# Optimization experiments

Measured on AMD Instinct MI355X. Metric: run time of the kernel, lower is better.

Reference implementation:

```python
import jax, jax.numpy as jnp
import numpy as np

B, S, C, E, H, D, V, K = 1024, 64, 512, 16, 1024, 256, 100, 2
NUM_NUM = 32  # num_numerical; categorical positions are S-NUM_NUM


def setup_inputs() -> dict:
    key = jax.random.key(0)
    ks = jax.random.split(key, 20)
    s = 0.02
    return {
        "codec": jax.random.normal(ks[0], (B, C), jnp.float32),
        "mask_pos": jax.random.randint(ks[1], (B, S), 0, 2, jnp.int32),
        "pos_emb": jax.random.normal(ks[2], (S, C), jnp.float32),
        "type_emb": jax.random.normal(ks[3], (2, C), jnp.float32),
        "gW1": jax.random.normal(ks[4], (3 * C + 1, 256), jnp.float32) * s,
        "gb1": jnp.zeros((256,), jnp.float32),
        "gW2": jax.random.normal(ks[5], (256, E), jnp.float32) * s,
        "gb2": jnp.zeros((E,), jnp.float32),
        "eW0": jax.random.normal(ks[6], (E, C, H), jnp.float32) * s,
        "eb0": jnp.zeros((E, H), jnp.float32),
        "eW1": jax.random.normal(ks[7], (E, H, H), jnp.float32) * s,
        "eb1": jnp.zeros((E, H), jnp.float32),
        "eW2": jax.random.normal(ks[8], (E, H, D), jnp.float32) * s,
        "eb2": jnp.zeros((E, D), jnp.float32),
        "nW": jax.random.normal(ks[9], (NUM_NUM, D), jnp.float32) * s,
        "nb": jnp.zeros((NUM_NUM,), jnp.float32),
        "cW": jax.random.normal(ks[10], (S - NUM_NUM, D, V), jnp.float32) * s,
        "cb": jnp.zeros((S - NUM_NUM, V), jnp.float32),
    }


def reference(codec, mask_pos, pos_emb, type_emb, gW1, gb1, gW2, gb2,
              eW0, eb0, eW1, eb1, eW2, eb2, nW, nb, cW, cb):
    maskf = mask_pos.astype(codec.dtype)  # [B,S]
    positions = jnp.arange(S)
    is_cat = (positions >= NUM_NUM).astype(jnp.int32)
    # gate input: [B,S,3C+1]
    gate_in = jnp.concatenate([
        jnp.broadcast_to(codec[:, None, :], (B, S, C)),
        jnp.broadcast_to(pos_emb[None], (B, S, C)),
        jnp.broadcast_to(type_emb[is_cat][None], (B, S, C)),
        maskf[..., None],
    ], axis=-1)
    h = jax.nn.gelu(gate_in @ gW1 + gb1, approximate=False)
    gate_logits = (h @ gW2 + gb2) * maskf[..., None]  # [B,S,E]
    topg, topi = jax.lax.top_k(gate_logits, K)  # [B,S,K]
    gates = jax.nn.softmax(topg, axis=-1)
    # all expert outputs on codec: [E,B,D]
    h0 = jax.nn.leaky_relu(jnp.einsum('bc,ech->ebh', codec, eW0) + eb0[:, None, :])
    h1 = jax.nn.leaky_relu(jnp.einsum('ebh,ehg->ebg', h0, eW1) + eb1[:, None, :])
    eout = jnp.einsum('ebg,egd->ebd', h1, eW2) + eb2[:, None, :]
    # per-token gather: tok[b,s,k,:] = eout[topi[b,s,k], b, :]
    eout_b = eout.transpose(1, 0, 2)  # [B,E,D]
    tok = jnp.take_along_axis(eout_b[:, None, :, :], topi[..., None], axis=2)  # [B,S,K,D]
    combined = jnp.einsum('bsk,bskd->bsd', gates, tok)  # [B,S,D]
    num_recon = jnp.einsum('bnd,nd->bn', combined[:, :NUM_NUM], nW) + nb  # [B,32]
    cat_recon = jnp.einsum('bnd,ndv->bnv', combined[:, NUM_NUM:], cW) + cb  # [B,32,V]
    return num_recon, cat_recon, gates, topi, mask_pos
```

## Files before the change

kernel.cpp:

```cpp
#include <hip/hip_runtime.h>
#include <hip/hip_bf16.h>

typedef __bf16 bf16x8 __attribute__((ext_vector_type(8)));
typedef float f32x4 __attribute__((ext_vector_type(4)));

static constexpr int B_ = 1024, S_ = 64, C_ = 512, E_ = 16, H_ = 1024, D_ = 256, V_ = 100;
static constexpr int NUMN = 32;

__device__ __forceinline__ unsigned short f2bf(float f) {
  union { float f; unsigned u; } x; x.f = f;
  unsigned r = x.u + 0x7fffu + ((x.u >> 16) & 1u);
  return (unsigned short)(r >> 16);
}

__device__ __forceinline__ float erf_fast(float x) {
  float ax = fabsf(x);
  float t = 1.0f / fmaf(0.3275911f, ax, 1.0f);
  float p = fmaf(1.061405429f, t, -1.453152027f);
  p = fmaf(p, t, 1.421413741f);
  p = fmaf(p, t, -0.284496736f);
  p = fmaf(p, t, 0.254829592f);
  p = p * t;
  float e = 1.0f - p * __expf(-ax * ax);
  return copysignf(e, x);
}

__global__ __launch_bounds__(256) void k_codec_bf(const float* __restrict__ src,
                                                  unsigned short* __restrict__ dst, int n) {
  int i = blockIdx.x * 256 + threadIdx.x;
  if (i < n) dst[i] = f2bf(src[i]);
}

__global__ __launch_bounds__(256) void k_transpose_bf(const float* __restrict__ W,
                                                      unsigned short* __restrict__ WT,
                                                      int K, int N) {
  __shared__ float t[32][33];
  int e = blockIdx.z;
  const float* We = W + (size_t)e * K * N;
  unsigned short* Te = WT + (size_t)e * N * K;
  int n0 = blockIdx.x * 32, k0 = blockIdx.y * 32;
  int tx = threadIdx.x & 31, ty = threadIdx.x >> 5;
#pragma unroll
  for (int i = 0; i < 32; i += 8) t[ty + i][tx] = We[(size_t)(k0 + ty + i) * N + n0 + tx];
  __syncthreads();
#pragma unroll
  for (int i = 0; i < 32; i += 8)
    Te[(size_t)(n0 + ty + i) * K + k0 + tx] = f2bf(t[tx][ty + i]);
}

__global__ __launch_bounds__(256) void k_cwt(const float* __restrict__ cW,
                                             unsigned short* __restrict__ cwt) {
  __shared__ float t[32][33];
  int n = blockIdx.z;
  const float* src = cW + (size_t)n * D_ * V_;
  unsigned short* dst = cwt + (size_t)n * 128 * 256;
  int v0 = blockIdx.x * 32, d0 = blockIdx.y * 32;
  int tx = threadIdx.x & 31, ty = threadIdx.x >> 5;
#pragma unroll
  for (int i = 0; i < 32; i += 8) {
    int v = v0 + tx;
    t[ty + i][tx] = (v < V_) ? src[(size_t)(d0 + ty + i) * V_ + v] : 0.f;
  }
  __syncthreads();
#pragma unroll
  for (int i = 0; i < 32; i += 8)
    dst[(size_t)(v0 + ty + i) * 256 + d0 + tx] = f2bf(t[tx][ty + i]);
}

__global__ __launch_bounds__(256) void k_cvt64(const float* __restrict__ gW2,
                                               const float* __restrict__ gW1,
                                               double* __restrict__ w2d,
                                               double* __restrict__ w1ld,
                                               int* __restrict__ flagcnt) {
  int i = blockIdx.x * 256 + threadIdx.x;
  if (i < 4096) w2d[i] = (double)gW2[i];
  if (i < 256) w1ld[i] = (double)gW1[(size_t)(3 * C_) * 256 + i];
  if (i == 0) *flagcnt = 0;
}

__global__ __launch_bounds__(256) void k_codecpart(const float* __restrict__ codec,
                                                   const float* __restrict__ gW1,
                                                   double* __restrict__ cp) {
  int j = threadIdx.x, b = blockIdx.x;
  const float* cb = codec + (size_t)b * C_;
  double a0 = 0, a1 = 0, a2 = 0, a3 = 0;
  for (int k = 0; k < C_; k += 4) {
    a0 += (double)cb[k] * (double)gW1[(size_t)k * 256 + j];
    a1 += (double)cb[k + 1] * (double)gW1[(size_t)(k + 1) * 256 + j];
    a2 += (double)cb[k + 2] * (double)gW1[(size_t)(k + 2) * 256 + j];
    a3 += (double)cb[k + 3] * (double)gW1[(size_t)(k + 3) * 256 + j];
  }
  cp[(size_t)b * 256 + j] = (a0 + a1) + (a2 + a3);
}

__global__ __launch_bounds__(256) void k_postype_part(const float* __restrict__ pos_emb,
                                                      const float* __restrict__ type_emb,
                                                      const float* __restrict__ gW1,
                                                      double* __restrict__ pp) {
  int j = threadIdx.x;
  int s = blockIdx.x;
  int kc = blockIdx.y;
  int tt = (s >= NUMN) ? 1 : 0;
  double a0 = 0, a1 = 0;
  int k0 = kc * 32;
  for (int kk = 0; kk < 32; kk += 2) {
    int k = k0 + kk;
    a0 += (double)pos_emb[(size_t)s * C_ + k] * (double)gW1[(size_t)(C_ + k) * 256 + j] +
          (double)type_emb[(size_t)tt * C_ + k] * (double)gW1[(size_t)(2 * C_ + k) * 256 + j];
    a1 += (double)pos_emb[(size_t)s * C_ + k + 1] * (double)gW1[(size_t)(C_ + k + 1) * 256 + j] +
          (double)type_emb[(size_t)tt * C_ + k + 1] * (double)gW1[(size_t)(2 * C_ + k + 1) * 256 + j];
  }
  pp[((size_t)kc * 64 + s) * 256 + j] = a0 + a1;
}

__global__ __launch_bounds__(256) void k_postype_red(const double* __restrict__ pp,
                                                     const float* __restrict__ gb1,
                                                     double* __restrict__ ptT) {
  int j = threadIdx.x;
  int s = blockIdx.x;
  double acc = (double)gb1[j];
#pragma unroll
  for (int kc = 0; kc < 16; ++kc) acc += pp[((size_t)kc * 64 + s) * 256 + j];
  ptT[(size_t)j * 64 + s] = acc;
}

__global__ __launch_bounds__(256) void k_gate(const double* __restrict__ cp,
                                              const double* __restrict__ ptT,
                                              const float* __restrict__ gW2,
                                              const double* __restrict__ w1ld,
                                              const float* __restrict__ gb2,
                                              const int* __restrict__ mask,
                                              float* __restrict__ out_g,
                                              float* __restrict__ out_i,
                                              float* __restrict__ out_m,
                                              float* __restrict__ tg,
                                              int* __restrict__ ti,
                                              int* __restrict__ flagcnt,
                                              int* __restrict__ flaglist) {
  __shared__ float red[3][64][17];
  int b = blockIdx.x;
  int s = threadIdx.x & 63;
  int wv = __builtin_amdgcn_readfirstlane(threadIdx.x >> 6);
  int token = b * 64 + s;
  double mf = (double)mask[token];
  const double* cpb = cp + (size_t)b * 256;
  float acc[16];
#pragma unroll
  for (int e = 0; e < 16; ++e) acc[e] = 0.f;
#pragma unroll 2
  for (int jj = 0; jj < 64; ++jj) {
    int j = wv * 64 + jj;
    double xd = cpb[j] + ptT[(size_t)j * 64 + s] + mf * w1ld[j];
    float x = (float)xd;
    float ef = erf_fast(x * 0.70710678f);
    float h = 0.5f * x * (1.0f + ef);
    const float* w2 = gW2 + (size_t)j * 16;
#pragma unroll
    for (int e = 0; e < 16; ++e) acc[e] = fmaf(h, w2[e], acc[e]);
  }
  if (wv > 0) {
#pragma unroll
    for (int e = 0; e < 16; ++e) red[wv - 1][s][e] = acc[e];
  }
  __syncthreads();
  if (wv == 0) {
    double vp[16];
#pragma unroll
    for (int e = 0; e < 16; ++e)
      vp[e] = (double)((acc[e] + red[0][s][e]) + (red[1][s][e] + red[2][s][e])) + (double)gb2[e];
    double margin;
    if (mf == 0.0) {
      double mn = 1e300;
#pragma unroll
      for (int e = 0; e < 16; ++e) mn = fmin(mn, fabs(vp[e]));
      margin = mn;
    } else {
      double t1 = -1e300, t2 = -1e300, t3 = -1e300;
#pragma unroll
      for (int e = 0; e < 16; ++e) {
        double v = vp[e];
        if (v > t1) { t3 = t2; t2 = t1; t1 = v; }
        else if (v > t2) { t3 = t2; t2 = v; }
        else if (v > t3) { t3 = v; }
      }
      margin = fmin(t1 - t2, t2 - t3);
    }
    if (margin < 1e-4) {
      int idx = atomicAdd(flagcnt, 1);
      if (idx < 8192) flaglist[idx] = token;
    }
    double v1, v2;
    int i1, i2;
    if (mf == 0.0) {
      int idx[2];
      int c = 0;
      for (int e = 0; e < 16 && c < 2; ++e)
        if (vp[e] > 0.0) idx[c++] = e;
      for (int e = 0; e < 16 && c < 2; ++e)
        if (!(vp[e] > 0.0)) idx[c++] = e;
      i1 = idx[0];
      i2 = idx[1];
      v1 = 0.0;
      v2 = 0.0;
    } else {
      v1 = -1e300; v2 = -1e300; i1 = 0; i2 = 1;
#pragma unroll
      for (int e = 0; e < 16; ++e) {
        double v = vp[e];
        if (v > v1) { v2 = v1; i2 = i1; v1 = v; i1 = e; }
        else if (v > v2) { v2 = v; i2 = e; }
      }
    }
    double ex = exp(v2 - v1);
    double den = 1.0 + ex;
    float g1 = (float)(1.0 / den), g2 = (float)(ex / den);
    out_g[(size_t)token * 2] = g1;
    out_g[(size_t)token * 2 + 1] = g2;
    out_i[(size_t)token * 2] = (float)i1;
    out_i[(size_t)token * 2 + 1] = (float)i2;
    out_m[token] = (float)mf;
    tg[(size_t)token * 2] = g1;
    tg[(size_t)token * 2 + 1] = g2;
    ti[(size_t)token * 2] = i1;
    ti[(size_t)token * 2 + 1] = i2;
  }
}

__global__ __launch_bounds__(64) void k_gate_fix(const double* __restrict__ cp,
                                                 const double* __restrict__ ptT,
                                                 const double* __restrict__ w2d,
                                                 const double* __restrict__ w1ld,
                                                 const float* __restrict__ gb2,
                                                 const int* __restrict__ mask,
                                                 const int* __restrict__ flagcnt,
                                                 const int* __restrict__ flaglist,
                                                 float* __restrict__ out_g,
                                                 float* __restrict__ out_i,
                                                 float* __restrict__ out_m,
                                                 float* __restrict__ tg,
                                                 int* __restrict__ ti) {
  int cnt = *flagcnt;
  if (cnt > 8192) cnt = 8192;
  int lane = threadIdx.x;
  for (int fi = blockIdx.x; fi < cnt; fi += gridDim.x) {
    int token = flaglist[fi];
    int b = token >> 6, sf = token & 63;
    double mf = (double)mask[token];
    const double* cpb = cp + (size_t)b * 256;
    double facc[16];
#pragma unroll
    for (int e = 0; e < 16; ++e) facc[e] = 0.0;
#pragma unroll
    for (int jj = 0; jj < 4; ++jj) {
      int j = jj * 64 + lane;
      double x = cpb[j] + ptT[(size_t)j * 64 + sf] + mf * w1ld[j];
      double h = 0.5 * x * (1.0 + erf(x * 0.70710678118654752440));
      const double* w2 = w2d + (size_t)j * 16;
#pragma unroll
      for (int e = 0; e < 16; ++e) facc[e] += h * w2[e];
    }
#pragma unroll
    for (int off = 32; off >= 1; off >>= 1) {
#pragma unroll
      for (int e = 0; e < 16; ++e) facc[e] += __shfl_xor(facc[e], off, 64);
    }
    if (lane == 0) {
      double vp[16];
#pragma unroll
      for (int e = 0; e < 16; ++e) vp[e] = facc[e] + (double)gb2[e];
      double v1, v2;
      int i1, i2;
      if (mf == 0.0) {
        int idx[2];
        int c = 0;
        for (int e = 0; e < 16 && c < 2; ++e)
          if (vp[e] > 0.0) idx[c++] = e;
        for (int e = 0; e < 16 && c < 2; ++e)
          if (!(vp[e] > 0.0)) idx[c++] = e;
        i1 = idx[0];
        i2 = idx[1];
        v1 = 0.0;
        v2 = 0.0;
      } else {
        v1 = -1e300; v2 = -1e300; i1 = 0; i2 = 1;
#pragma unroll
        for (int e = 0; e < 16; ++e) {
          double v = vp[e];
          if (v > v1) { v2 = v1; i2 = i1; v1 = v; i1 = e; }
          else if (v > v2) { v2 = v; i2 = e; }
        }
      }
      double ex = exp(v2 - v1);
      double den = 1.0 + ex;
      float g1 = (float)(1.0 / den), g2 = (float)(ex / den);
      out_g[(size_t)token * 2] = g1;
      out_g[(size_t)token * 2 + 1] = g2;
      out_i[(size_t)token * 2] = (float)i1;
      out_i[(size_t)token * 2 + 1] = (float)i2;
      out_m[token] = (float)mf;
      tg[(size_t)token * 2] = g1;
      tg[(size_t)token * 2 + 1] = g2;
      ti[(size_t)token * 2] = i1;
      ti[(size_t)token * 2 + 1] = i2;
    }
  }
}

__global__ __launch_bounds__(512, 2) void k_gemm256(const unsigned short* __restrict__ A, size_t aStride,
                                                    const unsigned short* __restrict__ WT,
                                                    const float* __restrict__ bias,
                                                    unsigned short* __restrict__ Out,
                                                    int M, int N, int K) {
  extern __shared__ char lds[];
  char* sA = lds;
  char* sB = lds + 65536;
  int id = blockIdx.x + gridDim.x * (blockIdx.y + gridDim.y * blockIdx.z);
  int e = (id & 7) * 2 + ((id >> 3) & 1);
  int tile = id >> 4;
  int m0 = (tile & 3) * 256, n0 = (tile >> 2) * 256;
  const unsigned short* Ae = A + (size_t)e * aStride;
  const unsigned short* We = WT + (size_t)e * (size_t)N * K;
  int tid = threadIdx.x, lane = tid & 63, w = tid >> 6;
  int l15 = lane & 15, l4 = lane >> 4;
  int r = w >> 2;
  int cc = (w & 3) * 64;
  int hc = cc >> 7;
  int cr = cc & 127;
  f32x4 acc[2][4][4] = {};
  int nk = K >> 6;

  auto stageA = [&](int buf, int h, int kt) {
#pragma unroll
    for (int c = 0; c < 2; ++c) {
      int off = (tid + c * 512) * 16;
      int row = off >> 7;
      int ss = ((off >> 4) & 7) ^ (row & 7);
      const char* src = (const char*)(Ae + (size_t)(m0 + h * 128 + row) * K + kt * 64) + ss * 16;
      __builtin_amdgcn_global_load_lds((const __attribute__((address_space(1))) void*)src,
          (__attribute__((address_space(3))) void*)(sA + buf * 32768 + h * 16384 + off), 16, 0, 0);
    }
  };
  auto stageB = [&](int buf, int h, int kt) {
#pragma unroll
    for (int c = 0; c < 2; ++c) {
      int off = (tid + c * 512) * 16;
      int row = off >> 7;
      int ss = ((off >> 4) & 7) ^ (row & 7);
      const char* src = (const char*)(We + (size_t)(n0 + h * 128 + row) * K + kt * 64) + ss * 16;
      __builtin_amdgcn_global_load_lds((const __attribute__((address_space(1))) void*)src,
          (__attribute__((address_space(3))) void*)(sB + buf * 32768 + h * 16384 + off), 16, 0, 0);
    }
  };
  auto ldA = [&](int buf, int m2, int mi, int ks) {
    int hrow = m2 * 64 + mi * 16 + l15;
    int sp = (l4 + ks * 4) ^ (hrow & 7);
    return *(const bf16x8*)(sA + buf * 32768 + r * 16384 + hrow * 128 + sp * 16);
  };
  auto ldB = [&](int buf, int ni, int ks) {
    int hrow = cr + ni * 16 + l15;
    int sp = (l4 + ks * 4) ^ (hrow & 7);
    return *(const bf16x8*)(sB + buf * 32768 + hc * 16384 + hrow * 128 + sp * 16);
  };

  stageA(0, 0, 0); stageA(0, 1, 0); stageB(0, 0, 0); stageB(0, 1, 0);
  asm volatile("s_waitcnt vmcnt(0)" ::: "memory");
  __builtin_amdgcn_s_barrier();

  for (int t = 0; t < nk; ++t) {
    int cur = t & 1, nxt = cur ^ 1;
    if (t + 1 < nk) {
      stageA(nxt, 0, t + 1); stageA(nxt, 1, t + 1);
      stageB(nxt, 0, t + 1); stageB(nxt, 1, t + 1);
    }
#pragma unroll
    for (int ks = 0; ks < 2; ++ks) {
      bf16x8 bfr[4];
#pragma unroll
      for (int ni = 0; ni < 4; ++ni) bfr[ni] = ldB(cur, ni, ks);
#pragma unroll
      for (int m2 = 0; m2 < 2; ++m2) {
        bf16x8 afr[4];
#pragma unroll
        for (int mi = 0; mi < 4; ++mi) afr[mi] = ldA(cur, m2, mi, ks);
        __builtin_amdgcn_s_setprio(1);
#pragma unroll
        for (int mi = 0; mi < 4; ++mi)
#pragma unroll
          for (int ni = 0; ni < 4; ++ni)
            acc[m2][mi][ni] = __builtin_amdgcn_mfma_f32_16x16x32_bf16(afr[mi], bfr[ni], acc[m2][mi][ni], 0, 0, 0);
        __builtin_amdgcn_s_setprio(0);
      }
    }
    asm volatile("s_waitcnt vmcnt(0)" ::: "memory");
    __builtin_amdgcn_s_barrier();
  }

  size_t obase = (size_t)e * (size_t)M * N;
#pragma unroll
  for (int m2 = 0; m2 < 2; ++m2)
#pragma unroll
    for (int mi = 0; mi < 4; ++mi)
#pragma unroll
      for (int ni = 0; ni < 4; ++ni) {
        int col = n0 + cc + ni * 16 + l15;
        float bv = bias[(size_t)e * N + col];
#pragma unroll
        for (int j = 0; j < 4; ++j) {
          int row = m0 + r * 128 + m2 * 64 + mi * 16 + l4 * 4 + j;
          float v = acc[m2][mi][ni][j] + bv;
          v = (v > 0.f) ? v : 0.01f * v;
          Out[obase + (size_t)row * N + col] = f2bf(v);
        }
      }
}

template <int ACT, int OBF>
__global__ __launch_bounds__(256) void k_gemm(const unsigned short* __restrict__ A, size_t aStride,
                                              const unsigned short* __restrict__ WT,
                                              const float* __restrict__ bias,
                                              void* __restrict__ Out,
                                              int M, int N, int K) {
  __shared__ __align__(16) unsigned short sA[128 * 32];
  __shared__ __align__(16) unsigned short sB[128 * 32];
  int e = blockIdx.z;
  int m0 = blockIdx.x * 128, n0 = blockIdx.y * 128;
  const unsigned short* Ae = A + (size_t)e * aStride;
  const unsigned short* We = WT + (size_t)e * (size_t)N * K;
  int tid = threadIdx.x, lane = tid & 63, w = tid >> 6;
  int l15 = lane & 15, kh = (lane >> 4) * 8;
  int rsub = lane >> 2;
  int kk = (lane & 3) * 8;
  int wr = (w >> 1) * 64, wc = (w & 1) * 64;
  f32x4 acc[4][4] = {};
  int nk = K >> 5;

  auto stage = [&](int kt) {
#pragma unroll
    for (int c = 0; c < 2; ++c) {
      int chunk = w * 2 + c;
      int row = chunk * 16 + rsub;
      const unsigned short* ga = Ae + (size_t)(m0 + row) * K + kt * 32 + kk;
      __builtin_amdgcn_global_load_lds((const __attribute__((address_space(1))) void*)ga,
                                       (__attribute__((address_space(3))) void*)(&sA[chunk * 512]),
                                       16, 0, 0);
      const unsigned short* gb = We + (size_t)(n0 + row) * K + kt * 32 + kk;
      __builtin_amdgcn_global_load_lds((const __attribute__((address_space(1))) void*)gb,
                                       (__attribute__((address_space(3))) void*)(&sB[chunk * 512]),
                                       16, 0, 0);
    }
  };

  stage(0);
  for (int kt = 0; kt < nk; ++kt) {
    __syncthreads();
    bf16x8 a[4], bb[4];
#pragma unroll
    for (int mi = 0; mi < 4; ++mi)
      a[mi] = *(const bf16x8*)&sA[(wr + mi * 16 + l15) * 32 + kh];
#pragma unroll
    for (int ni = 0; ni < 4; ++ni)
      bb[ni] = *(const bf16x8*)&sB[(wc + ni * 16 + l15) * 32 + kh];
#pragma unroll
    for (int mi = 0; mi < 4; ++mi)
#pragma unroll
      for (int ni = 0; ni < 4; ++ni)
        acc[mi][ni] = __builtin_amdgcn_mfma_f32_16x16x32_bf16(a[mi], bb[ni], acc[mi][ni], 0, 0, 0);
    if (kt + 1 < nk) {
      __syncthreads();
      stage(kt + 1);
    }
  }

  unsigned short* outb = (unsigned short*)Out;
  float* outf = (float*)Out;
  size_t obase = (size_t)e * (size_t)M * N;
#pragma unroll
  for (int mi = 0; mi < 4; ++mi) {
#pragma unroll
    for (int ni = 0; ni < 4; ++ni) {
      int col = n0 + wc + ni * 16 + l15;
      float bv = bias[(size_t)e * N + col];
#pragma unroll
      for (int j = 0; j < 4; ++j) {
        int row = m0 + wr + mi * 16 + (lane >> 4) * 4 + j;
        float v = acc[mi][ni][j] + bv;
        if (ACT) v = (v > 0.f) ? v : 0.01f * v;
        if (OBF) outb[obase + (size_t)row * N + col] = f2bf(v);
        else outf[obase + (size_t)row * N + col] = v;
      }
    }
  }
}

__global__ __launch_bounds__(256) void k_comb(const float* __restrict__ eout,
                                              const float* __restrict__ tg,
                                              const int* __restrict__ ti,
                                              unsigned short* __restrict__ combbf) {
  int b = blockIdx.x, n = blockIdx.y, d = threadIdx.x;
  int tk = b * 64 + 32 + n;
  float g1 = tg[(size_t)tk * 2], g2 = tg[(size_t)tk * 2 + 1];
  int i1 = ti[(size_t)tk * 2], i2 = ti[(size_t)tk * 2 + 1];
  float v = g1 * eout[((size_t)i1 * B_ + b) * D_ + d] + g2 * eout[((size_t)i2 * B_ + b) * D_ + d];
  combbf[((size_t)n * B_ + b) * D_ + d] = f2bf(v);
}

__global__ __launch_bounds__(256) void k_catgemm(const unsigned short* __restrict__ combbf,
                                                 const unsigned short* __restrict__ cwt,
                                                 const float* __restrict__ cb,
                                                 float* __restrict__ out1) {
  __shared__ __align__(16) unsigned short sA[128 * 32];
  __shared__ __align__(16) unsigned short sB[128 * 32];
  int n = blockIdx.z;
  int m0 = blockIdx.x * 128;
  const unsigned short* Ae = combbf + (size_t)n * B_ * D_;
  const unsigned short* We = cwt + (size_t)n * 128 * 256;
  int tid = threadIdx.x, lane = tid & 63, w = tid >> 6;
  int l15 = lane & 15, kh = (lane >> 4) * 8;
  int rsub = lane >> 2;
  int kk = (lane & 3) * 8;
  int wr = (w >> 1) * 64, wc = (w & 1) * 64;
  f32x4 acc[4][4] = {};
  const int K = 256, nk = K >> 5;

  auto stage = [&](int kt) {
#pragma unroll
    for (int c = 0; c < 2; ++c) {
      int chunk = w * 2 + c;
      int row = chunk * 16 + rsub;
      const unsigned short* ga = Ae + (size_t)(m0 + row) * K + kt * 32 + kk;
      __builtin_amdgcn_global_load_lds((const __attribute__((address_space(1))) void*)ga,
                                       (__attribute__((address_space(3))) void*)(&sA[chunk * 512]),
                                       16, 0, 0);
      const unsigned short* gb = We + (size_t)row * K + kt * 32 + kk;
      __builtin_amdgcn_global_load_lds((const __attribute__((address_space(1))) void*)gb,
                                       (__attribute__((address_space(3))) void*)(&sB[chunk * 512]),
                                       16, 0, 0);
    }
  };

  stage(0);
  for (int kt = 0; kt < nk; ++kt) {
    __syncthreads();
    bf16x8 a[4], bb[4];
#pragma unroll
    for (int mi = 0; mi < 4; ++mi)
      a[mi] = *(const bf16x8*)&sA[(wr + mi * 16 + l15) * 32 + kh];
#pragma unroll
    for (int ni = 0; ni < 4; ++ni)
      bb[ni] = *(const bf16x8*)&sB[(wc + ni * 16 + l15) * 32 + kh];
#pragma unroll
    for (int mi = 0; mi < 4; ++mi)
#pragma unroll
      for (int ni = 0; ni < 4; ++ni)
        acc[mi][ni] = __builtin_amdgcn_mfma_f32_16x16x32_bf16(a[mi], bb[ni], acc[mi][ni], 0, 0, 0);
    if (kt + 1 < nk) {
      __syncthreads();
      stage(kt + 1);
    }
  }

#pragma unroll
  for (int mi = 0; mi < 4; ++mi) {
#pragma unroll
    for (int ni = 0; ni < 4; ++ni) {
      int col = wc + ni * 16 + l15;
      if (col < V_) {
        float bv = cb[(size_t)n * V_ + col];
#pragma unroll
        for (int j = 0; j < 4; ++j) {
          int row = m0 + wr + mi * 16 + (lane >> 4) * 4 + j;
          out1[((size_t)row * 32 + n) * V_ + col] = acc[mi][ni][j] + bv;
        }
      }
    }
  }
}

__global__ __launch_bounds__(256) void k_num(const float* __restrict__ eout,
                                             const float* __restrict__ nW,
                                             const float* __restrict__ nb,
                                             const float* __restrict__ tg,
                                             const int* __restrict__ ti,
                                             float* __restrict__ out0) {
  int b = blockIdx.x;
  int lane = threadIdx.x & 63;
  int wv = threadIdx.x >> 6;
#pragma unroll
  for (int q = 0; q < 8; ++q) {
    int n = wv * 8 + q;
    int tk = b * 64 + n;
    float g1 = tg[(size_t)tk * 2], g2 = tg[(size_t)tk * 2 + 1];
    int i1 = ti[(size_t)tk * 2], i2 = ti[(size_t)tk * 2 + 1];
    const float4* p1 = (const float4*)(eout + ((size_t)i1 * B_ + b) * D_);
    const float4* p2 = (const float4*)(eout + ((size_t)i2 * B_ + b) * D_);
    const float4* wp = (const float4*)(nW + (size_t)n * D_);
    float4 a = p1[lane], c = p2[lane], ww = wp[lane];
    float acc = fmaf(g1, a.x, g2 * c.x) * ww.x + fmaf(g1, a.y, g2 * c.y) * ww.y +
                fmaf(g1, a.z, g2 * c.z) * ww.z + fmaf(g1, a.w, g2 * c.w) * ww.w;
#pragma unroll
    for (int off = 32; off >= 1; off >>= 1) acc += __shfl_xor(acc, off, 64);
    if (lane == 0) out0[(size_t)b * 32 + n] = nb[n] + acc;
  }
}

extern "C" void kernel_launch(void* const* d_in, const int* in_sizes, int n_in,
                              void* d_out, int out_size, void* d_ws, size_t ws_size,
                              hipStream_t stream) {
  const float* codec = (const float*)d_in[0];
  const int* maskp = (const int*)d_in[1];
  const float* pos_emb = (const float*)d_in[2];
  const float* type_emb = (const float*)d_in[3];
  const float* gW1 = (const float*)d_in[4];
  const float* gb1 = (const float*)d_in[5];
  const float* gW2 = (const float*)d_in[6];
  const float* gb2 = (const float*)d_in[7];
  const float* eW0 = (const float*)d_in[8];
  const float* eb0 = (const float*)d_in[9];
  const float* eW1 = (const float*)d_in[10];
  const float* eb1 = (const float*)d_in[11];
  const float* eW2 = (const float*)d_in[12];
  const float* eb2 = (const float*)d_in[13];
  const float* nW = (const float*)d_in[14];
  const float* nb = (const float*)d_in[15];
  const float* cW = (const float*)d_in[16];
  const float* cb = (const float*)d_in[17];

  char* ws = (char*)d_ws;
  size_t o = 0;
  unsigned short* codecbf = (unsigned short*)(ws + o); o += (size_t)B_ * C_ * 2;
  size_t o_w0t = o;
  unsigned short* w0t = (unsigned short*)(ws + o); o += (size_t)E_ * H_ * C_ * 2;
  unsigned short* w1t = (unsigned short*)(ws + o); o += (size_t)E_ * H_ * H_ * 2;
  unsigned short* w2t = (unsigned short*)(ws + o); o += (size_t)E_ * D_ * H_ * 2;
  size_t o_h0 = o;
  unsigned short* h0 = (unsigned short*)(ws + o); o += (size_t)E_ * B_ * H_ * 2;
  unsigned short* h1 = (unsigned short*)(ws + o); o += (size_t)E_ * B_ * H_ * 2;
  double* cp = (double*)(ws + o); o += (size_t)B_ * 256 * 8;
  double* ptT = (double*)(ws + o); o += (size_t)S_ * 256 * 8;
  float* tg = (float*)(ws + o); o += (size_t)B_ * S_ * 2 * 4;
  int* ti = (int*)(ws + o); o += (size_t)B_ * S_ * 2 * 4;
  double* w2d = (double*)(ws + o); o += 4096 * 8;
  double* w1ld = (double*)(ws + o); o += 256 * 8;
  unsigned short* cwt = (unsigned short*)(ws + o); o += (size_t)32 * 128 * 256 * 2;
  double* pp = (double*)(ws + o); o += (size_t)16 * 64 * 256 * 8;
  int* flagcnt = (int*)(ws + o); o += 256;
  int* flaglist = (int*)(ws + o); o += 8192 * 4;
  float* eout = (float*)(ws + o_w0t);
  unsigned short* combbf = (unsigned short*)(ws + o_h0);

  float* out = (float*)d_out;
  float* out_num = out;
  float* out_cat = out + 32768;
  float* out_g = out + 32768 + 3276800;
  float* out_i = out_g + (size_t)B_ * S_ * 2;
  float* out_m = out_i + (size_t)B_ * S_ * 2;

  hipLaunchKernelGGL(k_codec_bf, dim3((B_ * C_) / 256), dim3(256), 0, stream, codec, codecbf, B_ * C_);
  hipLaunchKernelGGL(k_cvt64, dim3(16), dim3(256), 0, stream, gW2, gW1, w2d, w1ld, flagcnt);
  hipLaunchKernelGGL(k_transpose_bf, dim3(H_ / 32, C_ / 32, E_), dim3(256), 0, stream, eW0, w0t, C_, H_);
  hipLaunchKernelGGL(k_transpose_bf, dim3(H_ / 32, H_ / 32, E_), dim3(256), 0, stream, eW1, w1t, H_, H_);
  hipLaunchKernelGGL(k_transpose_bf, dim3(D_ / 32, H_ / 32, E_), dim3(256), 0, stream, eW2, w2t, H_, D_);
  hipLaunchKernelGGL(k_cwt, dim3(4, 8, 32), dim3(256), 0, stream, cW, cwt);
  hipLaunchKernelGGL(k_codecpart, dim3(B_), dim3(256), 0, stream, codec, gW1, cp);
  hipLaunchKernelGGL(k_postype_part, dim3(S_, 16), dim3(256), 0, stream, pos_emb, type_emb, gW1, pp);
  hipLaunchKernelGGL(k_postype_red, dim3(S_), dim3(256), 0, stream, pp, gb1, ptT);
  hipLaunchKernelGGL(k_gate, dim3(B_), dim3(256), 0, stream, cp, ptT, gW2, w1ld, gb2,
                     maskp, out_g, out_i, out_m, tg, ti, flagcnt, flaglist);
  hipLaunchKernelGGL(k_gate_fix, dim3(2048), dim3(64), 0, stream, cp, ptT, w2d, w1ld, gb2,
                     maskp, flagcnt, flaglist, out_g, out_i, out_m, tg, ti);
  hipLaunchKernelGGL(k_gemm256, dim3(4, 4, E_), dim3(512), 131072, stream,
                     codecbf, (size_t)0, w0t, eb0, h0, 1024, 1024, 512);
  hipLaunchKernelGGL(k_gemm256, dim3(4, 4, E_), dim3(512), 131072, stream,
                     h0, (size_t)(B_ * H_), w1t, eb1, h1, 1024, 1024, 1024);
  hipLaunchKernelGGL((k_gemm<0, 0>), dim3(8, 2, E_), dim3(256), 0, stream,
                     h1, (size_t)(B_ * H_), w2t, eb2, (void*)eout, 1024, 256, 1024);
  hipLaunchKernelGGL(k_comb, dim3(B_, 32), dim3(256), 0, stream, eout, tg, ti, combbf);
  hipLaunchKernelGGL(k_num, dim3(B_), dim3(256), 0, stream, eout, nW, nb, tg, ti, out_num);
  hipLaunchKernelGGL(k_catgemm, dim3(8, 1, 32), dim3(256), 0, stream, combbf, cwt, cb, out_cat);
}
```

Baseline: 230.0 us.

## Switch expert GEMM to triple-buffered K=32 pipeline with partial vmcnt waits

The 256x256 expert GEMM kernel now stages K-tiles of 32 instead of 64 and keeps three LDS buffers in flight, prefetching two tiles ahead. It waits with vmcnt(4) rather than draining all loads each iteration, so global-to-LDS copies can overlap MFMA work. LDS use falls from 128KB to 96KB and launch bounds change to one block per CU. The trade-off is twice as many barriers per K step and a swizzle pattern that only spans 4 slots, which may raise LDS bank conflicts.

```diff
diff --git a/kernel.cpp b/kernel.cpp
--- a/kernel.cpp
+++ b/kernel.cpp
@@ -306,14 +306,12 @@
   }
 }
 
-__global__ __launch_bounds__(512, 2) void k_gemm256(const unsigned short* __restrict__ A, size_t aStride,
+__global__ __launch_bounds__(512, 1) void k_gemm256(const unsigned short* __restrict__ A, size_t aStride,
                                                     const unsigned short* __restrict__ WT,
                                                     const float* __restrict__ bias,
                                                     unsigned short* __restrict__ Out,
                                                     int M, int N, int K) {
   extern __shared__ char lds[];
-  char* sA = lds;
-  char* sB = lds + 65536;
   int id = blockIdx.x + gridDim.x * (blockIdx.y + gridDim.y * blockIdx.z);
   int e = (id & 7) * 2 + ((id >> 3) & 1);
   int tile = id >> 4;
@@ -324,75 +322,71 @@
   int l15 = lane & 15, l4 = lane >> 4;
   int r = w >> 2;
   int cc = (w & 3) * 64;
-  int hc = cc >> 7;
-  int cr = cc & 127;
   f32x4 acc[2][4][4] = {};
-  int nk = K >> 6;
-
-  auto stageA = [&](int buf, int h, int kt) {
+  int nk = K >> 5;
+
+  auto stageA = [&](int buf, int kt) {
 #pragma unroll
     for (int c = 0; c < 2; ++c) {
       int off = (tid + c * 512) * 16;
-      int row = off >> 7;
-      int ss = ((off >> 4) & 7) ^ (row & 7);
-      const char* src = (const char*)(Ae + (size_t)(m0 + h * 128 + row) * K + kt * 64) + ss * 16;
+      int row = off >> 6;
+      int ss = ((off >> 4) & 3) ^ (row & 3);
+      const char* src = (const char*)(Ae + (size_t)(m0 + row) * K + kt * 32) + ss * 16;
       __builtin_amdgcn_global_load_lds((const __attribute__((address_space(1))) void*)src,
-          (__attribute__((address_space(3))) void*)(sA + buf * 32768 + h * 16384 + off), 16, 0, 0);
+          (__attribute__((address_space(3))) void*)(lds + buf * 32768 + off), 16, 0, 0);
     }
   };
-  auto stageB = [&](int buf, int h, int kt) {
+  auto stageB = [&](int buf, int kt) {
 #pragma unroll
     for (int c = 0; c < 2; ++c) {
       int off = (tid + c * 512) * 16;
-      int row = off >> 7;
-      int ss = ((off >> 4) & 7) ^ (row & 7);
-      const char* src = (const char*)(We + (size_t)(n0 + h * 128 + row) * K + kt * 64) + ss * 16;
+      int row = off >> 6;
+      int ss = ((off >> 4) & 3) ^ (row & 3);
+      const char* src = (const char*)(We + (size_t)(n0 + row) * K + kt * 32) + ss * 16;
       __builtin_amdgcn_global_load_lds((const __attribute__((address_space(1))) void*)src,
-          (__attribute__((address_space(3))) void*)(sB + buf * 32768 + h * 16384 + off), 16, 0, 0);
+          (__attribute__((address_space(3))) void*)(lds + buf * 32768 + 16384 + off), 16, 0, 0);
     }
   };
-  auto ldA = [&](int buf, int m2, int mi, int ks) {
-    int hrow = m2 * 64 + mi * 16 + l15;
-    int sp = (l4 + ks * 4) ^ (hrow & 7);
-    return *(const bf16x8*)(sA + buf * 32768 + r * 16384 + hrow * 128 + sp * 16);
+  auto ldA = [&](int buf, int m2, int mi) {
+    int hrow = r * 128 + m2 * 64 + mi * 16 + l15;
+    int sp = l4 ^ (hrow & 3);
+    return *(const bf16x8*)(lds + buf * 32768 + hrow * 64 + sp * 16);
   };
-  auto ldB = [&](int buf, int ni, int ks) {
-    int hrow = cr + ni * 16 + l15;
-    int sp = (l4 + ks * 4) ^ (hrow & 7);
-    return *(const bf16x8*)(sB + buf * 32768 + hc * 16384 + hrow * 128 + sp * 16);
+  auto ldB = [&](int buf, int ni) {
+    int hrow = cc + ni * 16 + l15;
+    int sp = l4 ^ (hrow & 3);
+    return *(const bf16x8*)(lds + buf * 32768 + 16384 + hrow * 64 + sp * 16);
   };
 
-  stageA(0, 0, 0); stageA(0, 1, 0); stageB(0, 0, 0); stageB(0, 1, 0);
-  asm volatile("s_waitcnt vmcnt(0)" ::: "memory");
-  __builtin_amdgcn_s_barrier();
+  stageA(0, 0); stageB(0, 0);
+  stageA(1, 1); stageB(1, 1);
 
   for (int t = 0; t < nk; ++t) {
-    int cur = t & 1, nxt = cur ^ 1;
-    if (t + 1 < nk) {
-      stageA(nxt, 0, t + 1); stageA(nxt, 1, t + 1);
-      stageB(nxt, 0, t + 1); stageB(nxt, 1, t + 1);
-    }
-#pragma unroll
-    for (int ks = 0; ks < 2; ++ks) {
-      bf16x8 bfr[4];
-#pragma unroll
-      for (int ni = 0; ni < 4; ++ni) bfr[ni] = ldB(cur, ni, ks);
-#pragma unroll
-      for (int m2 = 0; m2 < 2; ++m2) {
-        bf16x8 afr[4];
-#pragma unroll
-        for (int mi = 0; mi < 4; ++mi) afr[mi] = ldA(cur, m2, mi, ks);
-        __builtin_amdgcn_s_setprio(1);
-#pragma unroll
-        for (int mi = 0; mi < 4; ++mi)
-#pragma unroll
-          for (int ni = 0; ni < 4; ++ni)
-            acc[m2][mi][ni] = __builtin_amdgcn_mfma_f32_16x16x32_bf16(afr[mi], bfr[ni], acc[m2][mi][ni], 0, 0, 0);
-        __builtin_amdgcn_s_setprio(0);
-      }
-    }
-    asm volatile("s_waitcnt vmcnt(0)" ::: "memory");
+    int cb3 = t % 3;
+    if (t < nk - 1) asm volatile("s_waitcnt vmcnt(4)" ::: "memory");
+    else asm volatile("s_waitcnt vmcnt(0)" ::: "memory");
     __builtin_amdgcn_s_barrier();
+    bf16x8 bfr[4];
+#pragma unroll
+    for (int ni = 0; ni < 4; ++ni) bfr[ni] = ldB(cb3, ni);
+#pragma unroll
+    for (int m2 = 0; m2 < 2; ++m2) {
+      bf16x8 afr[4];
+#pragma unroll
+      for (int mi = 0; mi < 4; ++mi) afr[mi] = ldA(cb3, m2, mi);
+      __builtin_amdgcn_s_setprio(1);
+#pragma unroll
+      for (int mi = 0; mi < 4; ++mi)
+#pragma unroll
+        for (int ni = 0; ni < 4; ++ni)
+          acc[m2][mi][ni] = __builtin_amdgcn_mfma_f32_16x16x32_bf16(afr[mi], bfr[ni], acc[m2][mi][ni], 0, 0, 0);
+      __builtin_amdgcn_s_setprio(0);
+    }
+    if (t + 2 < nk) {
+      int nb3 = (t + 2) % 3;
+      stageA(nb3, t + 2);
+      stageB(nb3, t + 2);
+    }
   }
 
   size_t obase = (size_t)e * (size_t)M * N;
@@ -668,9 +662,9 @@
                      maskp, out_g, out_i, out_m, tg, ti, flagcnt, flaglist);
   hipLaunchKernelGGL(k_gate_fix, dim3(2048), dim3(64), 0, stream, cp, ptT, w2d, w1ld, gb2,
                      maskp, flagcnt, flaglist, out_g, out_i, out_m, tg, ti);
-  hipLaunchKernelGGL(k_gemm256, dim3(4, 4, E_), dim3(512), 131072, stream,
+  hipLaunchKernelGGL(k_gemm256, dim3(4, 4, E_), dim3(512), 98304, stream,
                      codecbf, (size_t)0, w0t, eb0, h0, 1024, 1024, 512);
-  hipLaunchKernelGGL(k_gemm256, dim3(4, 4, E_), dim3(512), 131072, stream,
+  hipLaunchKernelGGL(k_gemm256, dim3(4, 4, E_), dim3(512), 98304, stream,
                      h0, (size_t)(B_ * H_), w1t, eb1, h1, 1024, 1024, 1024);
   hipLaunchKernelGGL((k_gemm<0, 0>), dim3(8, 2, E_), dim3(256), 0, stream,
                      h1, (size_t)(B_ * H_), w2t, eb2, (void*)eout, 1024, 256, 1024);
```

After: 232.7 us. Within noise of the previous version (+1.1%).
